# Kernel tuning notes

Measured on AMD Instinct MI355X. Metric: run time of the kernel, lower is better.

Reference implementation:

```python
import math
from itertools import combinations
import jax, jax.numpy as jnp
import numpy as np

SEQ_LEN = 8
D_IN = 2048
D_OUT = 1152
TSS = 3          # temporal_set_size
WAY = 5
SHOT = 5
N_SUPPORT = WAY * SHOT
N_Q = 100
PE_SCALE = 0.1
LN_EPS = 1e-5

TUPLES = np.array(list(combinations(range(SEQ_LEN), TSS)), dtype=np.int32)  # [56, 3]
T_LEN = TUPLES.shape[0]  # 56


def _positional_encoding(seq_len, d):
    pos = np.arange(seq_len, dtype=np.float32)[:, None]
    div = np.exp(np.arange(0, d, 2, dtype=np.float32) * -(math.log(10000.0) / d))
    pe = np.zeros((seq_len, d), dtype=np.float32)
    pe[:, 0::2] = np.sin(pos * div) * PE_SCALE
    pe[:, 1::2] = np.cos(pos * div) * PE_SCALE
    return jnp.asarray(pe)


def _layernorm(x, g, b):
    mu = jnp.mean(x, axis=-1, keepdims=True)
    var = jnp.mean((x - mu) ** 2, axis=-1, keepdims=True)
    return (x - mu) * jax.lax.rsqrt(var + LN_EPS) * g + b


def setup_inputs() -> dict:
    key = jax.random.key(0)
    ks = jax.random.split(key, 6)
    support_set = jax.random.normal(ks[0], (N_SUPPORT, SEQ_LEN, D_IN), dtype=jnp.float32)
    queries = jax.random.normal(ks[1], (N_Q, SEQ_LEN, D_IN), dtype=jnp.float32)
    # sorted episode layout: class c occupies rows [c*SHOT, (c+1)*SHOT)
    support_labels = jnp.repeat(jnp.arange(WAY, dtype=jnp.int64), SHOT)
    d_flat = TSS * D_IN  # 6144
    k_w = jax.random.normal(ks[2], (d_flat, D_OUT), dtype=jnp.float32) * 0.02
    k_b = jnp.zeros((D_OUT,), dtype=jnp.float32)
    v_w = jax.random.normal(ks[3], (d_flat, D_OUT), dtype=jnp.float32) * 0.02
    v_b = jnp.zeros((D_OUT,), dtype=jnp.float32)
    ln_g = jnp.ones((D_OUT,), dtype=jnp.float32)
    ln_b = jnp.zeros((D_OUT,), dtype=jnp.float32)
    return {"support_set": support_set, "queries": queries,
            "support_labels": support_labels,
            "k_w": k_w, "k_b": k_b, "v_w": v_w, "v_b": v_b,
            "ln_g": ln_g, "ln_b": ln_b}


def reference(support_set, queries, support_labels, k_w, k_b, v_w, v_b, ln_g, ln_b):
    pe = _positional_encoding(SEQ_LEN, D_IN)  # dropout is identity in eval mode
    s = support_set + pe
    q = queries + pe

    def tuplify(x):  # [N, S, D] -> [N, T_LEN, TSS*D]
        return x[:, TUPLES, :].reshape(x.shape[0], T_LEN, TSS * D_IN)

    s_t = tuplify(s)
    q_t = tuplify(q)

    sk = _layernorm(s_t @ k_w + k_b, ln_g, ln_b)  # [25, 56, 1152]
    qk = _layernorm(q_t @ k_w + k_b, ln_g, ln_b)  # [100, 56, 1152]
    sv = s_t @ v_w + v_b                           # [25, 56, 1152]
    qv = q_t @ v_w + v_b                           # [100, 56, 1152]

    scale = 1.0 / math.sqrt(D_OUT)
    dists = []
    align = None
    for c in range(WAY):  # fixed small class loop; class rows are a static slice
        class_k = sk[c * SHOT:(c + 1) * SHOT]  # [SHOT, 56, 1152]
        class_v = sv[c * SHOT:(c + 1) * SHOT]
        # scores: [Q, T, K, T] == torch permute(0,2,1,3) of [Q, K, T, T]
        scores = jnp.einsum('qtd,ksd->qtks', qk, class_k) * scale
        flat = scores.reshape(N_Q, T_LEN, SHOT * T_LEN)
        sm = jax.nn.softmax(flat, axis=-1)
        sm = sm.reshape(N_Q, T_LEN, SHOT, T_LEN).transpose(0, 2, 1, 3)  # [Q, K, T, T]
        align = sm.sum(axis=1)  # [Q, T, T]
        proto = jnp.einsum('qkts,ksd->qtd', sm, class_v)  # [Q, 56, 1152]
        diff = qv - proto
        dists.append(-jnp.sum(diff * diff, axis=(-2, -1)) / T_LEN)  # [Q]
    logits = jnp.stack(dists, axis=1)  # [Q, WAY]
    return logits, align
```

## Files before the change

### kernel.cpp

```cpp
#include <hip/hip_runtime.h>
#include <hip/hip_bf16.h>
#include <math.h>

#define SEQ_LEN 8
#define D_IN 2048
#define D_OUT 1152
#define WAY 5
#define SHOT 5
#define N_SUPPORT 25
#define N_Q 100
#define N_SEQ 125
#define N_ROWS 1000
#define T_LEN 56
#define KS_LEN 280
#define KS_PAD 288
#define NCOLS 6912
#define MQT 5600
#define DPC 9

typedef __attribute__((ext_vector_type(4))) float f32x4;
typedef __attribute__((ext_vector_type(8))) short bf16x8;

__constant__ int TUP[T_LEN][3] = {
  {0,1,2},{0,1,3},{0,1,4},{0,1,5},{0,1,6},{0,1,7},{0,2,3},{0,2,4},{0,2,5},{0,2,6},
  {0,2,7},{0,3,4},{0,3,5},{0,3,6},{0,3,7},{0,4,5},{0,4,6},{0,4,7},{0,5,6},{0,5,7},
  {0,6,7},{1,2,3},{1,2,4},{1,2,5},{1,2,6},{1,2,7},{1,3,4},{1,3,5},{1,3,6},{1,3,7},
  {1,4,5},{1,4,6},{1,4,7},{1,5,6},{1,5,7},{1,6,7},{2,3,4},{2,3,5},{2,3,6},{2,3,7},
  {2,4,5},{2,4,6},{2,4,7},{2,5,6},{2,5,7},{2,6,7},{3,4,5},{3,4,6},{3,4,7},{3,5,6},
  {3,5,7},{3,6,7},{4,5,6},{4,5,7},{4,6,7},{5,6,7}
};

__device__ __forceinline__ ushort f2bf(float f) {
  union { float f; unsigned u; } v; v.f = f;
  unsigned r = v.u + 0x7FFFu + ((v.u >> 16) & 1u);
  return (ushort)(r >> 16);
}
__device__ __forceinline__ float bf2f(ushort u) {
  union { unsigned u; float f; } v; v.u = ((unsigned)u) << 16;
  return v.f;
}
__device__ __forceinline__ void gload16(const void* g, const void* l) {
  __builtin_amdgcn_global_load_lds(
      (const __attribute__((address_space(1))) unsigned int*)g,
      (__attribute__((address_space(3))) unsigned int*)l, 16, 0, 0);
}
template<int N> __device__ __forceinline__ void vmw() {
  asm volatile("s_waitcnt vmcnt(%0)" :: "n"(N) : "memory");
}
__device__ __forceinline__ void vmw_rt(int n) {
  switch (n) {
    case 0: vmw<0>(); break;
    case 3: vmw<3>(); break;
    case 4: vmw<4>(); break;
    case 6: vmw<6>(); break;
    case 8: vmw<8>(); break;
    case 9: vmw<9>(); break;
    case 12: vmw<12>(); break;
    case 16: vmw<16>(); break;
    default: vmw<0>(); break;
  }
}

__global__ __launch_bounds__(256) void pe_table(float* __restrict__ PE) {
  int idx = blockIdx.x * 256 + threadIdx.x;
  if (idx >= SEQ_LEN * D_IN) return;
  int d = idx & (D_IN - 1), i = idx >> 11;
  int h2 = d & ~1;
  float freq = expf((float)h2 * (-9.210340371976184f / (float)D_IN));
  float ang = (float)i * freq;
  PE[idx] = ((d & 1) ? cosf(ang) : sinf(ang)) * 0.1f;
}

__global__ __launch_bounds__(256) void pe_add4(const float* __restrict__ sup,
                                               const float* __restrict__ que,
                                               const float* __restrict__ PE,
                                               ushort* __restrict__ X) {
  int idx = blockIdx.x * 256 + threadIdx.x;
  if (idx >= N_ROWS * D_IN / 4) return;
  int d4 = idx & (D_IN / 4 - 1);
  int r = idx >> 9;
  int i = r & 7;
  float4 p = *(const float4*)(PE + (size_t)i * D_IN + d4 * 4);
  float4 v = (r < N_SUPPORT * SEQ_LEN)
                 ? *(const float4*)(sup + (size_t)idx * 4)
                 : *(const float4*)(que + (size_t)idx * 4 - (size_t)N_SUPPORT * SEQ_LEN * D_IN);
  ushort4 o;
  o.x = f2bf(v.x + p.x); o.y = f2bf(v.y + p.y);
  o.z = f2bf(v.z + p.z); o.w = f2bf(v.w + p.w);
  *(ushort4*)(X + (size_t)idx * 4) = o;
}

__global__ __launch_bounds__(256) void wtrans(const float* __restrict__ kw,
                                              const float* __restrict__ vw,
                                              ushort* __restrict__ WT) {
  __shared__ float tile[64][65];
  int bx = blockIdx.x;
  int by = blockIdx.y;
  int b = bx / 18;
  int n0 = (bx % 18) * 64;
  int k0 = by * 64;
  const float* src = ((b & 1) ? vw : kw) + (size_t)(b >> 1) * D_IN * D_OUT;
  int tid = threadIdx.x;
#pragma unroll
  for (int it = 0; it < 4; ++it) {
    int lin4 = it * 256 + tid;
    int kk = lin4 >> 4;
    int n4 = (lin4 & 15) * 4;
    float4 v = *(const float4*)(src + (size_t)(k0 + kk) * D_OUT + n0 + n4);
    tile[kk][n4 + 0] = v.x; tile[kk][n4 + 1] = v.y;
    tile[kk][n4 + 2] = v.z; tile[kk][n4 + 3] = v.w;
  }
  __syncthreads();
#pragma unroll
  for (int it = 0; it < 4; ++it) {
    int lin = it * 1024 + tid * 4;
    int nn = lin >> 6, kk = lin & 63;
    ushort4 o;
    o.x = f2bf(tile[kk + 0][nn]); o.y = f2bf(tile[kk + 1][nn]);
    o.z = f2bf(tile[kk + 2][nn]); o.w = f2bf(tile[kk + 3][nn]);
    *(ushort4*)&WT[((size_t)(b * D_OUT + n0 + nn)) * D_IN + k0 + kk] = o;
  }
}

template<int EPI, int NT, int DEPTH, int SWZ>
__global__ __launch_bounds__(256) void gemm_bt(
    const ushort* __restrict__ A, const ushort* __restrict__ BT,
    float* __restrict__ C,
    int M, int N, int K, int lda, int ldb, int ldc, float alpha,
    long batchA, long batchB, long batchC) {
  constexpr int JF = NT / 32;
  constexpr int NCH = 8 + NT / 16;
  __shared__ ushort As[DEPTH][128][32];
  __shared__ ushort Bs[DEPTH][NT][32];

  int bx, by, bz;
  if constexpr (SWZ == 1) {
    int L = blockIdx.x, xcd = L & 7, s = L >> 3;
    by = (s >> 3) * 8 + xcd;
    if (by >= 108) return;
    bx = s & 7; bz = 0;
  } else if constexpr (SWZ == 2) {
    int L = blockIdx.x, xcd = L & 7, s = L >> 3;
    bx = (s % 6) * 8 + xcd;
    if (bx >= 44) return;
    int g = s / 6; by = g % 3; bz = g / 3;
  } else { bx = blockIdx.x; by = blockIdx.y; bz = blockIdx.z; }

  A  += (size_t)bz * batchA;
  BT += (size_t)bz * batchB;
  C  += (size_t)bz * batchC;

  int tid = threadIdx.x;
  int wid = tid >> 6, lane = tid & 63;
  int l16 = lane & 15, lk = lane >> 4;
  int wr = wid >> 1, wc = wid & 1;
  int row0 = bx * 128, col0 = by * NT;
  int lrow = lane >> 2;
  int lcol = ((lane & 3) ^ ((lane >> 3) & 3)) * 8;
  int rslot = (lk ^ ((l16 >> 1) & 3)) * 8;

  auto stage = [&](int buf, int t) {
    int k0 = t * 32;
    for (int c = wid; c < NCH; c += 4) {
      if (c < 8) {
        int grow = row0 + c * 16 + lrow;
        grow = grow < M ? grow : M - 1;
        gload16(A + (size_t)grow * lda + k0 + lcol, &As[buf][c * 16][0]);
      } else {
        int gcol = col0 + (c - 8) * 16 + lrow;
        gcol = gcol < N ? gcol : N - 1;
        gload16(BT + (size_t)gcol * ldb + k0 + lcol, &Bs[buf][(c - 8) * 16][0]);
      }
    }
  };

  int perw = NCH / 4 + ((wid < (NCH & 3)) ? 1 : 0);
  f32x4 acc[4][JF] = {};
  int nk = K / 32;
#pragma unroll
  for (int i = 0; i < DEPTH - 1; ++i)
    if (i < nk) stage(i, i);
  for (int t = 0; t < nk; ++t) {
    int cur = t % DEPTH;
    int ts = t + DEPTH - 1;
    if (ts < nk) stage(ts % DEPTH, ts);
    int rem = nk - 1 - t; if (rem > DEPTH - 1) rem = DEPTH - 1;
    vmw_rt(rem * perw);
    __builtin_amdgcn_s_barrier();
    __builtin_amdgcn_sched_barrier(0);
    bf16x8 af[4], bv[JF];
#pragma unroll
    for (int m = 0; m < 4; ++m)
      af[m] = *(const bf16x8*)&As[cur][wr * 64 + m * 16 + l16][rslot];
#pragma unroll
    for (int j = 0; j < JF; ++j)
      bv[j] = *(const bf16x8*)&Bs[cur][wc * (NT / 2) + j * 16 + l16][rslot];
#pragma unroll
    for (int m = 0; m < 4; ++m)
#pragma unroll
      for (int j = 0; j < JF; ++j)
        acc[m][j] = __builtin_amdgcn_mfma_f32_16x16x32_bf16(af[m], bv[j], acc[m][j], 0, 0, 0);
    __builtin_amdgcn_sched_barrier(0);
    __builtin_amdgcn_s_barrier();
  }

#pragma unroll
  for (int m = 0; m < 4; ++m)
#pragma unroll
    for (int j = 0; j < JF; ++j) {
      int col = col0 + wc * (NT / 2) + j * 16 + l16;
#pragma unroll
      for (int r = 0; r < 4; ++r) {
        int row = row0 + wr * 64 + m * 16 + lk * 4 + r;
        if (row < M && col < N)
          C[(size_t)row * ldc + col] = (EPI == 1) ? acc[m][j][r] * alpha : acc[m][j][r];
      }
    }
}

__global__ __launch_bounds__(256) void pv_dist(const ushort* __restrict__ SM,
                                               const ushort* __restrict__ SVT,
                                               const ushort* __restrict__ QV,
                                               float* __restrict__ DP) {
  __shared__ ushort Bs[128][296];
  int L = blockIdx.x, xcd = L & 7, s = L >> 3;
  int bx = (s % 6) * 8 + xcd;
  if (bx >= 44) return;
  int g = s / 6; int by = g % 9, bz = g / 9;
  int tid = threadIdx.x, wid = tid >> 6, lane = tid & 63;
  int l16 = lane & 15, lk = lane >> 4;
  int row0 = bx * 128, col0 = by * 128, c = bz;
  const ushort* sm = SM + (size_t)c * MQT * KS_PAD;
  const ushort* bt = SVT + ((size_t)c * D_OUT + col0) * KS_PAD;
  {
    int r = tid >> 1, h = tid & 1;
    const ushort* srcr = bt + (size_t)r * KS_PAD + h * 144;
#pragma unroll
    for (int i = 0; i < 18; ++i) {
      uint4 v = *(const uint4*)(srcr + i * 8);
      *(uint4*)&Bs[r][h * 144 + i * 8] = v;
    }
  }
  __syncthreads();

  int ra0 = row0 + wid * 32 + l16;      if (ra0 > MQT - 1) ra0 = MQT - 1;
  int ra1 = row0 + wid * 32 + 16 + l16; if (ra1 > MQT - 1) ra1 = MQT - 1;
  const ushort* a0 = sm + (size_t)ra0 * KS_PAD + lk * 8;
  const ushort* a1 = sm + (size_t)ra1 * KS_PAD + lk * 8;

  f32x4 acc[2][8] = {};
#pragma unroll
  for (int ks = 0; ks < 9; ++ks) {
    bf16x8 af0 = *(const bf16x8*)(a0 + ks * 32);
    bf16x8 af1 = *(const bf16x8*)(a1 + ks * 32);
    bf16x8 bv[8];
#pragma unroll
    for (int j = 0; j < 8; ++j)
      bv[j] = *(const bf16x8*)&Bs[j * 16 + l16][ks * 32 + lk * 8];
#pragma unroll
    for (int j = 0; j < 8; ++j) {
      acc[0][j] = __builtin_amdgcn_mfma_f32_16x16x32_bf16(af0, bv[j], acc[0][j], 0, 0, 0);
      acc[1][j] = __builtin_amdgcn_mfma_f32_16x16x32_bf16(af1, bv[j], acc[1][j], 0, 0, 0);
    }
  }

  float sq[2][4] = {};
#pragma unroll
  for (int m = 0; m < 2; ++m)
#pragma unroll
    for (int r = 0; r < 4; ++r) {
      int row = row0 + wid * 32 + m * 16 + lk * 4 + r;
      int rowc = row < MQT ? row : MQT - 1;
      const ushort* qvr = QV + (size_t)rowc * D_OUT + col0;
#pragma unroll
      for (int j = 0; j < 8; ++j) {
        float qvv = bf2f(qvr[j * 16 + l16]);
        float d = qvv - acc[m][j][r];
        sq[m][r] += d * d;
      }
    }
#pragma unroll
  for (int m = 0; m < 2; ++m)
#pragma unroll
    for (int r = 0; r < 4; ++r) {
      sq[m][r] += __shfl_xor(sq[m][r], 1);
      sq[m][r] += __shfl_xor(sq[m][r], 2);
      sq[m][r] += __shfl_xor(sq[m][r], 4);
      sq[m][r] += __shfl_xor(sq[m][r], 8);
    }
  if (l16 == 0) {
    float* dp = DP + (size_t)c * MQT * DPC;
#pragma unroll
    for (int m = 0; m < 2; ++m)
#pragma unroll
      for (int r = 0; r < 4; ++r) {
        int row = row0 + wid * 32 + m * 16 + lk * 4 + r;
        if (row < MQT) dp[(size_t)row * DPC + by] = sq[m][r];
      }
  }
}

__global__ __launch_bounds__(256) void combine_ln(const float* __restrict__ G,
                                                  const float* __restrict__ kb,
                                                  const float* __restrict__ vb,
                                                  const float* __restrict__ lng,
                                                  const float* __restrict__ lnb,
                                                  ushort* __restrict__ skbf,
                                                  ushort* __restrict__ qkbf,
                                                  ushort* __restrict__ sv,
                                                  ushort* __restrict__ qvbf) {
  int L = blockIdx.x, xcd = L & 7, h = L >> 3;
  int n = (h / 14) * 8 + xcd;
  if (n >= N_SEQ) return;
  int t = (h % 14) * 4 + (threadIdx.x >> 6);
  int lane = threadIdx.x & 63;
  const float* g0 = G + (size_t)(n * 8 + TUP[t][0]) * NCOLS;
  const float* g1 = G + (size_t)(n * 8 + TUP[t][1]) * NCOLS + 2 * D_OUT;
  const float* g2 = G + (size_t)(n * 8 + TUP[t][2]) * NCOLS + 4 * D_OUT;
  bool isq = (n >= N_SUPPORT);
  int c = n / SHOT, s = n % SHOT;
  ushort* vout = isq ? qvbf + ((size_t)(n - N_SUPPORT) * T_LEN + t) * D_OUT
                     : sv + ((size_t)c * KS_PAD + s * T_LEN + t) * D_OUT;
  ushort* kout = isq ? qkbf + ((size_t)(n - N_SUPPORT) * T_LEN + t) * D_OUT
                     : skbf + ((size_t)c * KS_PAD + s * T_LEN + t) * D_OUT;
  float kvx[9], kvy[9], s1 = 0.f, s2 = 0.f;
#pragma unroll
  for (int i = 0; i < 9; ++i) {
    int d = i * 128 + lane * 2;
    float2 a = *(const float2*)(g0 + d);
    float2 b = *(const float2*)(g0 + D_OUT + d);
    float2 c1 = *(const float2*)(g1 + d);
    float2 c2 = *(const float2*)(g1 + D_OUT + d);
    float2 e1 = *(const float2*)(g2 + d);
    float2 e2 = *(const float2*)(g2 + D_OUT + d);
    float2 kb2 = *(const float2*)(kb + d);
    float2 vb2 = *(const float2*)(vb + d);
    float kx = a.x + c1.x + e1.x + kb2.x;
    float ky = a.y + c1.y + e1.y + kb2.y;
    float vx = b.x + c2.x + e2.x + vb2.x;
    float vy = b.y + c2.y + e2.y + vb2.y;
    kvx[i] = kx; kvy[i] = ky;
    ushort2 vv; vv.x = f2bf(vx); vv.y = f2bf(vy);
    *(ushort2*)(vout + d) = vv;
    s1 += kx + ky;
    s2 += kx * kx + ky * ky;
  }
#pragma unroll
  for (int m = 32; m > 0; m >>= 1) {
    s1 += __shfl_xor(s1, m);
    s2 += __shfl_xor(s2, m);
  }
  float mu = s1 * (1.0f / D_OUT);
  float var = s2 * (1.0f / D_OUT) - mu * mu;
  float rs = rsqrtf(var + 1e-5f);
#pragma unroll
  for (int i = 0; i < 9; ++i) {
    int d = i * 128 + lane * 2;
    float2 g2v = *(const float2*)(lng + d);
    float2 b2v = *(const float2*)(lnb + d);
    ushort2 o;
    o.x = f2bf((kvx[i] - mu) * rs * g2v.x + b2v.x);
    o.y = f2bf((kvy[i] - mu) * rs * g2v.y + b2v.y);
    *(ushort2*)(kout + d) = o;
  }
}

__global__ __launch_bounds__(256) void svtrans(const ushort* __restrict__ sv,
                                               ushort* __restrict__ svT) {
  __shared__ ushort tile[32][65];
  int c = blockIdx.z;
  int d0 = blockIdx.x * 64;
  int k0 = blockIdx.y * 32;
  const ushort* src = sv + (size_t)c * KS_PAD * D_OUT;
  ushort* dst = svT + (size_t)c * D_OUT * KS_PAD;
  int tid = threadIdx.x;
#pragma unroll
  for (int it = 0; it < 8; ++it) {
    int lin = it * 256 + tid;
    int ks = k0 + (lin >> 6), d = d0 + (lin & 63);
    tile[lin >> 6][lin & 63] = (ks < KS_LEN) ? src[(size_t)ks * D_OUT + d] : (ushort)0;
  }
  __syncthreads();
#pragma unroll
  for (int it = 0; it < 8; ++it) {
    int lin = it * 256 + tid;
    int d = lin >> 5, ks = lin & 31;
    dst[(size_t)(d0 + d) * KS_PAD + k0 + ks] = tile[ks][d];
  }
}

__global__ __launch_bounds__(256) void softmax_align(const float* __restrict__ S,
                                                     ushort* __restrict__ sm,
                                                     float* __restrict__ align_out) {
  __shared__ float pl[4][KS_LEN];
  int wid = threadIdx.x >> 6, lane = threadIdx.x & 63;
  int row = blockIdx.x * 4 + wid;
  const float* src = S + (size_t)row * KS_PAD;
  float v[5];
  float mx = -1e30f;
#pragma unroll
  for (int j = 0; j < 5; ++j) {
    int ks = lane + j * 64;
    v[j] = (ks < KS_LEN) ? src[ks] : -1e30f;
    mx = fmaxf(mx, v[j]);
  }
#pragma unroll
  for (int m = 32; m > 0; m >>= 1) mx = fmaxf(mx, __shfl_xor(mx, m));
  float sum = 0.f;
  float p[5];
#pragma unroll
  for (int j = 0; j < 5; ++j) {
    int ks = lane + j * 64;
    p[j] = (ks < KS_LEN) ? expf(v[j] - mx) : 0.f;
    sum += p[j];
  }
#pragma unroll
  for (int m = 32; m > 0; m >>= 1) sum += __shfl_xor(sum, m);
  float inv = 1.0f / sum;
  ushort* dst = sm + (size_t)row * KS_PAD;
#pragma unroll
  for (int j = 0; j < 5; ++j) {
    int ks = lane + j * 64;
    if (ks < KS_PAD) dst[ks] = f2bf((ks < KS_LEN) ? p[j] * inv : 0.f);
  }
  int c = row / MQT;
  if (c == WAY - 1) {
#pragma unroll
    for (int j = 0; j < 5; ++j) {
      int ks = lane + j * 64;
      if (ks < KS_LEN) pl[wid][ks] = p[j] * inv;
    }
    __syncthreads();
    if (lane < T_LEN) {
      float a = 0.f;
#pragma unroll
      for (int k = 0; k < SHOT; ++k) a += pl[wid][k * T_LEN + lane];
      int qt = row - (WAY - 1) * MQT;
      align_out[(size_t)(qt / T_LEN) * (T_LEN * T_LEN) + (qt % T_LEN) * T_LEN + lane] = a;
    }
  }
}

__global__ __launch_bounds__(256) void logits_k(const float* __restrict__ DP,
                                                float* __restrict__ out) {
  __shared__ float red[256];
  int q = blockIdx.x / WAY, c = blockIdx.x % WAY;
  const float* base = DP + ((size_t)c * MQT + q * T_LEN) * DPC;
  int tid = threadIdx.x;
  float s = 0.f;
  for (int i = tid; i < T_LEN * DPC; i += 256) s += base[i];
  red[tid] = s;
  __syncthreads();
  for (int sft = 128; sft > 0; sft >>= 1) {
    if (tid < sft) red[tid] += red[tid + sft];
    __syncthreads();
  }
  if (tid == 0) out[blockIdx.x] = -red[0] * (1.0f / T_LEN);
}

extern "C" void kernel_launch(void* const* d_in, const int* in_sizes, int n_in,
                              void* d_out, int out_size, void* d_ws, size_t ws_size,
                              hipStream_t stream) {
  const float* sup  = (const float*)d_in[0];
  const float* que  = (const float*)d_in[1];
  const float* k_w  = (const float*)d_in[3];
  const float* k_b  = (const float*)d_in[4];
  const float* v_w  = (const float*)d_in[5];
  const float* v_b  = (const float*)d_in[6];
  const float* ln_g = (const float*)d_in[7];
  const float* ln_b = (const float*)d_in[8];
  float* out = (float*)d_out;

  char* w = (char*)d_ws;
  ushort* Xbf  = (ushort*)(w + 0);
  float*  PEt  = (float*)(w + 4096000);
  ushort* WT   = (ushort*)(w + 4096000);
  float*  G    = (float*)(w + 32407552);
  ushort* sv   = (ushort*)(w + 0);
  float*  S    = (float*)(w + 0);
  ushort* smbf = (ushort*)(w + 32407552);
  float*  DP   = (float*)(w + 0);
  ushort* qkbf = (ushort*)(w + 60055552);
  ushort* skbf = (ushort*)(w + 72957952);
  ushort* svT  = (ushort*)(w + 76275712);
  ushort* qvbf = (ushort*)(w + 79593472);

  const float scale = 0.02946278254943948f;

  pe_table<<<dim3(64), 256, 0, stream>>>(PEt);
  pe_add4<<<dim3(2000), 256, 0, stream>>>(sup, que, PEt, Xbf);
  wtrans<<<dim3(108, 32), 256, 0, stream>>>(k_w, v_w, WT);
  gemm_bt<0, 64, 3, 1><<<dim3(896), 256, 0, stream>>>(
      Xbf, WT, G,
      N_ROWS, NCOLS, D_IN, D_IN, D_IN, NCOLS, 1.0f, 0, 0, 0);
  combine_ln<<<dim3(1792), 256, 0, stream>>>(
      G, k_b, v_b, ln_g, ln_b, skbf, qkbf, sv, qvbf);
  svtrans<<<dim3(18, 9, WAY), 256, 0, stream>>>(sv, svT);
  gemm_bt<1, 96, 3, 2><<<dim3(720), 256, 0, stream>>>(
      qkbf, skbf, S,
      MQT, KS_PAD, D_OUT, D_OUT, D_OUT, KS_PAD, scale,
      0, (long)KS_PAD * D_OUT, (long)MQT * KS_PAD);
  softmax_align<<<dim3(7000), 256, 0, stream>>>(S, smbf, out + N_Q * WAY);
  pv_dist<<<dim3(2160), 256, 0, stream>>>(smbf, svT, qvbf, DP);
  logits_k<<<dim3(N_Q * WAY), 256, 0, stream>>>(DP, out);
}
```

Baseline: 203.2 us.

## Fuse score GEMM with softmax and align; compute positional encoding inline

Replaces the separate scores GEMM and softmax_align kernels with one kernel. Each block computes a full 64x288 row tile of scores, then does the row softmax in registers through cross-wave shared-memory max/sum reductions, writes bf16 probabilities, and computes align for the last class. This removes the fp32 score matrix round trip through global memory and one launch. The PE table kernel is also dropped in favour of computing sin/cos inline in pe_add4. The fused kernel runs only 440 blocks with a wide per-block N tile, which may lower occupancy relative to the old 720-block GEMM.

```diff
diff --git a/kernel.cpp b/kernel.cpp
--- a/kernel.cpp
+++ b/kernel.cpp
@@ -52,6 +52,7 @@
     case 0: vmw<0>(); break;
     case 3: vmw<3>(); break;
     case 4: vmw<4>(); break;
+    case 5: vmw<5>(); break;
     case 6: vmw<6>(); break;
     case 8: vmw<8>(); break;
     case 9: vmw<9>(); break;
@@ -61,32 +62,27 @@
   }
 }
 
-__global__ __launch_bounds__(256) void pe_table(float* __restrict__ PE) {
-  int idx = blockIdx.x * 256 + threadIdx.x;
-  if (idx >= SEQ_LEN * D_IN) return;
-  int d = idx & (D_IN - 1), i = idx >> 11;
-  int h2 = d & ~1;
-  float freq = expf((float)h2 * (-9.210340371976184f / (float)D_IN));
-  float ang = (float)i * freq;
-  PE[idx] = ((d & 1) ? cosf(ang) : sinf(ang)) * 0.1f;
-}
-
 __global__ __launch_bounds__(256) void pe_add4(const float* __restrict__ sup,
                                                const float* __restrict__ que,
-                                               const float* __restrict__ PE,
                                                ushort* __restrict__ X) {
   int idx = blockIdx.x * 256 + threadIdx.x;
   if (idx >= N_ROWS * D_IN / 4) return;
   int d4 = idx & (D_IN / 4 - 1);
   int r = idx >> 9;
   int i = r & 7;
-  float4 p = *(const float4*)(PE + (size_t)i * D_IN + d4 * 4);
+  int d = d4 * 4;
+  const float C = -9.210340371976184f / (float)D_IN;
+  float f0 = expf((float)d * C);
+  float f1 = expf((float)(d + 2) * C);
+  float s0, c0, s1, c1;
+  sincosf((float)i * f0, &s0, &c0);
+  sincosf((float)i * f1, &s1, &c1);
   float4 v = (r < N_SUPPORT * SEQ_LEN)
                  ? *(const float4*)(sup + (size_t)idx * 4)
                  : *(const float4*)(que + (size_t)idx * 4 - (size_t)N_SUPPORT * SEQ_LEN * D_IN);
   ushort4 o;
-  o.x = f2bf(v.x + p.x); o.y = f2bf(v.y + p.y);
-  o.z = f2bf(v.z + p.z); o.w = f2bf(v.w + p.w);
+  o.x = f2bf(v.x + s0 * 0.1f); o.y = f2bf(v.y + c0 * 0.1f);
+  o.z = f2bf(v.z + s1 * 0.1f); o.w = f2bf(v.w + c1 * 0.1f);
   *(ushort4*)(X + (size_t)idx * 4) = o;
 }
 
@@ -139,11 +135,6 @@
     by = (s >> 3) * 8 + xcd;
     if (by >= 108) return;
     bx = s & 7; bz = 0;
-  } else if constexpr (SWZ == 2) {
-    int L = blockIdx.x, xcd = L & 7, s = L >> 3;
-    bx = (s % 6) * 8 + xcd;
-    if (bx >= 44) return;
-    int g = s / 6; by = g % 3; bz = g / 3;
   } else { bx = blockIdx.x; by = blockIdx.y; bz = blockIdx.z; }
 
   A  += (size_t)bz * batchA;
@@ -216,6 +207,172 @@
           C[(size_t)row * ldc + col] = (EPI == 1) ? acc[m][j][r] * alpha : acc[m][j][r];
       }
     }
+}
+
+__global__ __launch_bounds__(256) void scores_sm(const ushort* __restrict__ QK,
+                                                 const ushort* __restrict__ SK,
+                                                 ushort* __restrict__ SM,
+                                                 float* __restrict__ align_out) {
+  __shared__ ushort AsB[2][64][32];
+  __shared__ ushort BsB[2][288][32];
+  __shared__ float pmax[64][2];
+  __shared__ float psum[64][2];
+  int L = blockIdx.x, xcd = L & 7, s = L >> 3;
+  int bx = (s % 11) * 8 + xcd;
+  int cz = s / 11;
+  const ushort* B = SK + (size_t)cz * KS_PAD * D_OUT;
+  ushort* smc = SM + (size_t)cz * MQT * KS_PAD;
+  int row0 = bx * 64;
+
+  int tid = threadIdx.x;
+  int wid = tid >> 6, lane = tid & 63;
+  int l16 = lane & 15, lk = lane >> 4;
+  int wr = wid >> 1, wc = wid & 1;
+  int lrow = lane >> 2;
+  int lcol = ((lane & 3) ^ ((lane >> 3) & 3)) * 8;
+  int rslot = (lk ^ ((l16 >> 1) & 3)) * 8;
+
+  auto stage = [&](int buf, int t) {
+    int k0 = t * 32;
+    for (int c = wid; c < 22; c += 4) {
+      if (c < 4) {
+        int grow = row0 + c * 16 + lrow;
+        grow = grow < MQT ? grow : MQT - 1;
+        gload16(QK + (size_t)grow * D_OUT + k0 + lcol, &AsB[buf][c * 16][0]);
+      } else {
+        int gcol = (c - 4) * 16 + lrow;
+        gcol = gcol < KS_LEN ? gcol : KS_LEN - 1;
+        gload16(B + (size_t)gcol * D_OUT + k0 + lcol, &BsB[buf][(c - 4) * 16][0]);
+      }
+    }
+  };
+
+  int perw = (wid < 2) ? 6 : 5;
+  f32x4 acc[2][9] = {};
+  stage(0, 0);
+  for (int t = 0; t < 36; ++t) {
+    int cur = t & 1;
+    if (t + 1 < 36) {
+      stage(cur ^ 1, t + 1);
+      vmw_rt(perw);
+    } else {
+      vmw<0>();
+    }
+    __builtin_amdgcn_s_barrier();
+    __builtin_amdgcn_sched_barrier(0);
+    bf16x8 af[2], bv[9];
+#pragma unroll
+    for (int m = 0; m < 2; ++m)
+      af[m] = *(const bf16x8*)&AsB[cur][wr * 32 + m * 16 + l16][rslot];
+#pragma unroll
+    for (int j = 0; j < 9; ++j)
+      bv[j] = *(const bf16x8*)&BsB[cur][wc * 144 + j * 16 + l16][rslot];
+#pragma unroll
+    for (int m = 0; m < 2; ++m)
+#pragma unroll
+      for (int j = 0; j < 9; ++j)
+        acc[m][j] = __builtin_amdgcn_mfma_f32_16x16x32_bf16(af[m], bv[j], acc[m][j], 0, 0, 0);
+    __builtin_amdgcn_sched_barrier(0);
+    __builtin_amdgcn_s_barrier();
+  }
+
+  const float scale = 0.02946278254943948f;
+  float mxv[2][4];
+#pragma unroll
+  for (int m = 0; m < 2; ++m)
+#pragma unroll
+    for (int r = 0; r < 4; ++r) {
+      float mx = -1e30f;
+#pragma unroll
+      for (int j = 0; j < 9; ++j) {
+        acc[m][j][r] *= scale;
+        int col = wc * 144 + j * 16 + l16;
+        if (col < KS_LEN) mx = fmaxf(mx, acc[m][j][r]);
+      }
+      mx = fmaxf(mx, __shfl_xor(mx, 1));
+      mx = fmaxf(mx, __shfl_xor(mx, 2));
+      mx = fmaxf(mx, __shfl_xor(mx, 4));
+      mx = fmaxf(mx, __shfl_xor(mx, 8));
+      mxv[m][r] = mx;
+    }
+  __syncthreads();
+  if (l16 == 0) {
+#pragma unroll
+    for (int m = 0; m < 2; ++m)
+#pragma unroll
+      for (int r = 0; r < 4; ++r)
+        pmax[wr * 32 + m * 16 + lk * 4 + r][wc] = mxv[m][r];
+  }
+  __syncthreads();
+  float smv[2][4];
+#pragma unroll
+  for (int m = 0; m < 2; ++m)
+#pragma unroll
+    for (int r = 0; r < 4; ++r) {
+      int lr = wr * 32 + m * 16 + lk * 4 + r;
+      float mx = fmaxf(pmax[lr][0], pmax[lr][1]);
+      float sum = 0.f;
+#pragma unroll
+      for (int j = 0; j < 9; ++j) {
+        int col = wc * 144 + j * 16 + l16;
+        float p = (col < KS_LEN) ? expf(acc[m][j][r] - mx) : 0.f;
+        acc[m][j][r] = p;
+        sum += p;
+      }
+      sum += __shfl_xor(sum, 1);
+      sum += __shfl_xor(sum, 2);
+      sum += __shfl_xor(sum, 4);
+      sum += __shfl_xor(sum, 8);
+      smv[m][r] = sum;
+    }
+  if (l16 == 0) {
+#pragma unroll
+    for (int m = 0; m < 2; ++m)
+#pragma unroll
+      for (int r = 0; r < 4; ++r)
+        psum[wr * 32 + m * 16 + lk * 4 + r][wc] = smv[m][r];
+  }
+  __syncthreads();
+#pragma unroll
+  for (int m = 0; m < 2; ++m)
+#pragma unroll
+    for (int r = 0; r < 4; ++r) {
+      int lr = wr * 32 + m * 16 + lk * 4 + r;
+      int row = row0 + lr;
+      float inv = 1.0f / (psum[lr][0] + psum[lr][1]);
+#pragma unroll
+      for (int j = 0; j < 9; ++j) {
+        acc[m][j][r] *= inv;
+        int col = wc * 144 + j * 16 + l16;
+        if (row < MQT) smc[(size_t)row * KS_PAD + col] = f2bf(acc[m][j][r]);
+      }
+    }
+  if (cz == WAY - 1) {
+    ushort* sml = &BsB[0][0][0];
+    __syncthreads();
+#pragma unroll
+    for (int m = 0; m < 2; ++m)
+#pragma unroll
+      for (int r = 0; r < 4; ++r) {
+        int lr = wr * 32 + m * 16 + lk * 4 + r;
+#pragma unroll
+        for (int j = 0; j < 9; ++j) {
+          int col = wc * 144 + j * 16 + l16;
+          sml[lr * 288 + col] = f2bf(acc[m][j][r]);
+        }
+      }
+    __syncthreads();
+    for (int idx = tid; idx < 64 * T_LEN; idx += 256) {
+      int lr = idx / T_LEN, s5 = idx % T_LEN;
+      int grow = row0 + lr;
+      if (grow < MQT) {
+        float a = 0.f;
+#pragma unroll
+        for (int k = 0; k < SHOT; ++k) a += bf2f(sml[lr * 288 + k * T_LEN + s5]);
+        align_out[(size_t)(grow / T_LEN) * (T_LEN * T_LEN) + (grow % T_LEN) * T_LEN + s5] = a;
+      }
+    }
+  }
 }
 
 __global__ __launch_bounds__(256) void pv_dist(const ushort* __restrict__ SM,
@@ -389,58 +546,6 @@
   }
 }
 
-__global__ __launch_bounds__(256) void softmax_align(const float* __restrict__ S,
-                                                     ushort* __restrict__ sm,
-                                                     float* __restrict__ align_out) {
-  __shared__ float pl[4][KS_LEN];
-  int wid = threadIdx.x >> 6, lane = threadIdx.x & 63;
-  int row = blockIdx.x * 4 + wid;
-  const float* src = S + (size_t)row * KS_PAD;
-  float v[5];
-  float mx = -1e30f;
-#pragma unroll
-  for (int j = 0; j < 5; ++j) {
-    int ks = lane + j * 64;
-    v[j] = (ks < KS_LEN) ? src[ks] : -1e30f;
-    mx = fmaxf(mx, v[j]);
-  }
-#pragma unroll
-  for (int m = 32; m > 0; m >>= 1) mx = fmaxf(mx, __shfl_xor(mx, m));
-  float sum = 0.f;
-  float p[5];
-#pragma unroll
-  for (int j = 0; j < 5; ++j) {
-    int ks = lane + j * 64;
-    p[j] = (ks < KS_LEN) ? expf(v[j] - mx) : 0.f;
-    sum += p[j];
-  }
-#pragma unroll
-  for (int m = 32; m > 0; m >>= 1) sum += __shfl_xor(sum, m);
-  float inv = 1.0f / sum;
-  ushort* dst = sm + (size_t)row * KS_PAD;
-#pragma unroll
-  for (int j = 0; j < 5; ++j) {
-    int ks = lane + j * 64;
-    if (ks < KS_PAD) dst[ks] = f2bf((ks < KS_LEN) ? p[j] * inv : 0.f);
-  }
-  int c = row / MQT;
-  if (c == WAY - 1) {
-#pragma unroll
-    for (int j = 0; j < 5; ++j) {
-      int ks = lane + j * 64;
-      if (ks < KS_LEN) pl[wid][ks] = p[j] * inv;
-    }
-    __syncthreads();
-    if (lane < T_LEN) {
-      float a = 0.f;
-#pragma unroll
-      for (int k = 0; k < SHOT; ++k) a += pl[wid][k * T_LEN + lane];
-      int qt = row - (WAY - 1) * MQT;
-      align_out[(size_t)(qt / T_LEN) * (T_LEN * T_LEN) + (qt % T_LEN) * T_LEN + lane] = a;
-    }
-  }
-}
-
 __global__ __launch_bounds__(256) void logits_k(const float* __restrict__ DP,
                                                 float* __restrict__ out) {
   __shared__ float red[256];
@@ -473,11 +578,9 @@
 
   char* w = (char*)d_ws;
   ushort* Xbf  = (ushort*)(w + 0);
-  float*  PEt  = (float*)(w + 4096000);
   ushort* WT   = (ushort*)(w + 4096000);
   float*  G    = (float*)(w + 32407552);
   ushort* sv   = (ushort*)(w + 0);
-  float*  S    = (float*)(w + 0);
   ushort* smbf = (ushort*)(w + 32407552);
   float*  DP   = (float*)(w + 0);
   ushort* qkbf = (ushort*)(w + 60055552);
@@ -485,10 +588,7 @@
   ushort* svT  = (ushort*)(w + 76275712);
   ushort* qvbf = (ushort*)(w + 79593472);
 
-  const float scale = 0.02946278254943948f;
-
-  pe_table<<<dim3(64), 256, 0, stream>>>(PEt);
-  pe_add4<<<dim3(2000), 256, 0, stream>>>(sup, que, PEt, Xbf);
+  pe_add4<<<dim3(2000), 256, 0, stream>>>(sup, que, Xbf);
   wtrans<<<dim3(108, 32), 256, 0, stream>>>(k_w, v_w, WT);
   gemm_bt<0, 64, 3, 1><<<dim3(896), 256, 0, stream>>>(
       Xbf, WT, G,
@@ -496,11 +596,7 @@
   combine_ln<<<dim3(1792), 256, 0, stream>>>(
       G, k_b, v_b, ln_g, ln_b, skbf, qkbf, sv, qvbf);
   svtrans<<<dim3(18, 9, WAY), 256, 0, stream>>>(sv, svT);
-  gemm_bt<1, 96, 3, 2><<<dim3(720), 256, 0, stream>>>(
-      qkbf, skbf, S,
-      MQT, KS_PAD, D_OUT, D_OUT, D_OUT, KS_PAD, scale,
-      0, (long)KS_PAD * D_OUT, (long)MQT * KS_PAD);
-  softmax_align<<<dim3(7000), 256, 0, stream>>>(S, smbf, out + N_Q * WAY);
+  scores_sm<<<dim3(440), 256, 0, stream>>>(qkbf, skbf, smbf, out + N_Q * WAY);
   pv_dist<<<dim3(2160), 256, 0, stream>>>(smbf, svT, qvbf, DP);
   logits_k<<<dim3(N_Q * WAY), 256, 0, stream>>>(DP, out);
 }
```

Result: faster. 195.5 us (-3.8%).

## Replace QK score GEMM with LDS-resident support-key kernel and inline PE computation

Applied to the files above, without the earlier changes.

Swaps the generic pipelined GEMM for the query-key scores with a dedicated kernel. Each block keeps a 32-row slice of the class's support keys (full 1152 depth) in LDS and streams query rows straight from global memory into MFMA, with no K-loop staging or barriers. It also drops the separate positional-encoding table kernel and computes sin/cos inline in pe_add4, removing one launch and a table read. The risks are uncached direct global loads of A with many more blocks re-reading the query rows, and about 74KB of LDS per block, which limits occupancy.

```diff
diff --git a/kernel.cpp b/kernel.cpp
--- a/kernel.cpp
+++ b/kernel.cpp
@@ -52,6 +52,7 @@
     case 0: vmw<0>(); break;
     case 3: vmw<3>(); break;
     case 4: vmw<4>(); break;
+    case 5: vmw<5>(); break;
     case 6: vmw<6>(); break;
     case 8: vmw<8>(); break;
     case 9: vmw<9>(); break;
@@ -61,32 +62,27 @@
   }
 }
 
-__global__ __launch_bounds__(256) void pe_table(float* __restrict__ PE) {
-  int idx = blockIdx.x * 256 + threadIdx.x;
-  if (idx >= SEQ_LEN * D_IN) return;
-  int d = idx & (D_IN - 1), i = idx >> 11;
-  int h2 = d & ~1;
-  float freq = expf((float)h2 * (-9.210340371976184f / (float)D_IN));
-  float ang = (float)i * freq;
-  PE[idx] = ((d & 1) ? cosf(ang) : sinf(ang)) * 0.1f;
-}
-
 __global__ __launch_bounds__(256) void pe_add4(const float* __restrict__ sup,
                                                const float* __restrict__ que,
-                                               const float* __restrict__ PE,
                                                ushort* __restrict__ X) {
   int idx = blockIdx.x * 256 + threadIdx.x;
   if (idx >= N_ROWS * D_IN / 4) return;
   int d4 = idx & (D_IN / 4 - 1);
   int r = idx >> 9;
   int i = r & 7;
-  float4 p = *(const float4*)(PE + (size_t)i * D_IN + d4 * 4);
+  int d = d4 * 4;
+  const float C = -9.210340371976184f / (float)D_IN;
+  float f0 = expf((float)d * C);
+  float f1 = expf((float)(d + 2) * C);
+  float s0, c0, s1, c1;
+  sincosf((float)i * f0, &s0, &c0);
+  sincosf((float)i * f1, &s1, &c1);
   float4 v = (r < N_SUPPORT * SEQ_LEN)
                  ? *(const float4*)(sup + (size_t)idx * 4)
                  : *(const float4*)(que + (size_t)idx * 4 - (size_t)N_SUPPORT * SEQ_LEN * D_IN);
   ushort4 o;
-  o.x = f2bf(v.x + p.x); o.y = f2bf(v.y + p.y);
-  o.z = f2bf(v.z + p.z); o.w = f2bf(v.w + p.w);
+  o.x = f2bf(v.x + s0 * 0.1f); o.y = f2bf(v.y + c0 * 0.1f);
+  o.z = f2bf(v.z + s1 * 0.1f); o.w = f2bf(v.w + c1 * 0.1f);
   *(ushort4*)(X + (size_t)idx * 4) = o;
 }
 
@@ -139,11 +135,6 @@
     by = (s >> 3) * 8 + xcd;
     if (by >= 108) return;
     bx = s & 7; bz = 0;
-  } else if constexpr (SWZ == 2) {
-    int L = blockIdx.x, xcd = L & 7, s = L >> 3;
-    bx = (s % 6) * 8 + xcd;
-    if (bx >= 44) return;
-    int g = s / 6; by = g % 3; bz = g / 3;
   } else { bx = blockIdx.x; by = blockIdx.y; bz = blockIdx.z; }
 
   A  += (size_t)bz * batchA;
@@ -216,6 +207,112 @@
           C[(size_t)row * ldc + col] = (EPI == 1) ? acc[m][j][r] * alpha : acc[m][j][r];
       }
     }
+}
+
+__global__ __launch_bounds__(256) void qk_scores(const ushort* __restrict__ QK,
+                                                 const ushort* __restrict__ SK,
+                                                 float* __restrict__ S) {
+  __shared__ ushort Bs[32][1160];
+  int L = blockIdx.x, xcd = L & 7, s = L >> 3;
+  int bx = (s % 6) * 8 + xcd;
+  if (bx >= 44) return;
+  int g = s / 6; int by = g % 9, bz = g / 9;
+  int tid = threadIdx.x, wid = tid >> 6, lane = tid & 63;
+  int l16 = lane & 15, lk = lane >> 4;
+  int row0 = bx * 128, ks0 = by * 32, c = bz;
+  const ushort* skc = SK + ((size_t)c * KS_PAD + ks0) * D_OUT;
+  {
+    int r = tid >> 3, h = tid & 7;
+    const ushort* srcr = skc + (size_t)r * D_OUT + h * 144;
+#pragma unroll
+    for (int i = 0; i < 18; ++i)
+      *(uint4*)&Bs[r][h * 144 + i * 8] = *(const uint4*)(srcr + i * 8);
+  }
+  __syncthreads();
+
+  int ra0 = row0 + wid * 32 + l16;      if (ra0 > MQT - 1) ra0 = MQT - 1;
+  int ra1 = row0 + wid * 32 + 16 + l16; if (ra1 > MQT - 1) ra1 = MQT - 1;
+  const ushort* a0 = QK + (size_t)ra0 * D_OUT + lk * 8;
+  const ushort* a1 = QK + (size_t)ra1 * D_OUT + lk * 8;
+
+  f32x4 acc[2][2] = {};
+#pragma unroll 4
+  for (int t = 0; t < 36; ++t) {
+    bf16x8 af0 = *(const bf16x8*)(a0 + t * 32);
+    bf16x8 af1 = *(const bf16x8*)(a1 + t * 32);
+    bf16x8 bv0 = *(const bf16x8*)&Bs[l16][t * 32 + lk * 8];
+    bf16x8 bv1 = *(const bf16x8*)&Bs[16 + l16][t * 32 + lk * 8];
+    acc[0][0] = __builtin_amdgcn_mfma_f32_16x16x32_bf16(af0, bv0, acc[0][0], 0, 0, 0);
+    acc[0][1] = __builtin_amdgcn_mfma_f32_16x16x32_bf16(af0, bv1, acc[0][1], 0, 0, 0);
+    acc[1][0] = __builtin_amdgcn_mfma_f32_16x16x32_bf16(af1, bv0, acc[1][0], 0, 0, 0);
+    acc[1][1] = __builtin_amdgcn_mfma_f32_16x16x32_bf16(af1, bv1, acc[1][1], 0, 0, 0);
+  }
+
+  const float scale = 0.02946278254943948f;
+  float* sc = S + (size_t)c * MQT * KS_PAD;
+#pragma unroll
+  for (int m = 0; m < 2; ++m)
+#pragma unroll
+    for (int j = 0; j < 2; ++j) {
+      int col = ks0 + j * 16 + l16;
+#pragma unroll
+      for (int r = 0; r < 4; ++r) {
+        int row = row0 + wid * 32 + m * 16 + lk * 4 + r;
+        if (row < MQT) sc[(size_t)row * KS_PAD + col] = acc[m][j][r] * scale;
+      }
+    }
+}
+
+__global__ __launch_bounds__(256) void softmax_align(const float* __restrict__ S,
+                                                     ushort* __restrict__ sm,
+                                                     float* __restrict__ align_out) {
+  __shared__ float pl[4][KS_LEN];
+  int wid = threadIdx.x >> 6, lane = threadIdx.x & 63;
+  int row = blockIdx.x * 4 + wid;
+  const float* src = S + (size_t)row * KS_PAD;
+  float v[5];
+  float mx = -1e30f;
+#pragma unroll
+  for (int j = 0; j < 5; ++j) {
+    int ks = lane + j * 64;
+    v[j] = (ks < KS_LEN) ? src[ks] : -1e30f;
+    mx = fmaxf(mx, v[j]);
+  }
+#pragma unroll
+  for (int m = 32; m > 0; m >>= 1) mx = fmaxf(mx, __shfl_xor(mx, m));
+  float sum = 0.f;
+  float p[5];
+#pragma unroll
+  for (int j = 0; j < 5; ++j) {
+    int ks = lane + j * 64;
+    p[j] = (ks < KS_LEN) ? expf(v[j] - mx) : 0.f;
+    sum += p[j];
+  }
+#pragma unroll
+  for (int m = 32; m > 0; m >>= 1) sum += __shfl_xor(sum, m);
+  float inv = 1.0f / sum;
+  ushort* dst = sm + (size_t)row * KS_PAD;
+#pragma unroll
+  for (int j = 0; j < 5; ++j) {
+    int ks = lane + j * 64;
+    if (ks < KS_PAD) dst[ks] = f2bf((ks < KS_LEN) ? p[j] * inv : 0.f);
+  }
+  int c = row / MQT;
+  if (c == WAY - 1) {
+#pragma unroll
+    for (int j = 0; j < 5; ++j) {
+      int ks = lane + j * 64;
+      if (ks < KS_LEN) pl[wid][ks] = p[j] * inv;
+    }
+    __syncthreads();
+    if (lane < T_LEN) {
+      float a = 0.f;
+#pragma unroll
+      for (int k = 0; k < SHOT; ++k) a += pl[wid][k * T_LEN + lane];
+      int qt = row - (WAY - 1) * MQT;
+      align_out[(size_t)(qt / T_LEN) * (T_LEN * T_LEN) + (qt % T_LEN) * T_LEN + lane] = a;
+    }
+  }
 }
 
 __global__ __launch_bounds__(256) void pv_dist(const ushort* __restrict__ SM,
@@ -389,58 +486,6 @@
   }
 }
 
-__global__ __launch_bounds__(256) void softmax_align(const float* __restrict__ S,
-                                                     ushort* __restrict__ sm,
-                                                     float* __restrict__ align_out) {
-  __shared__ float pl[4][KS_LEN];
-  int wid = threadIdx.x >> 6, lane = threadIdx.x & 63;
-  int row = blockIdx.x * 4 + wid;
-  const float* src = S + (size_t)row * KS_PAD;
-  float v[5];
-  float mx = -1e30f;
-#pragma unroll
-  for (int j = 0; j < 5; ++j) {
-    int ks = lane + j * 64;
-    v[j] = (ks < KS_LEN) ? src[ks] : -1e30f;
-    mx = fmaxf(mx, v[j]);
-  }
-#pragma unroll
-  for (int m = 32; m > 0; m >>= 1) mx = fmaxf(mx, __shfl_xor(mx, m));
-  float sum = 0.f;
-  float p[5];
-#pragma unroll
-  for (int j = 0; j < 5; ++j) {
-    int ks = lane + j * 64;
-    p[j] = (ks < KS_LEN) ? expf(v[j] - mx) : 0.f;
-    sum += p[j];
-  }
-#pragma unroll
-  for (int m = 32; m > 0; m >>= 1) sum += __shfl_xor(sum, m);
-  float inv = 1.0f / sum;
-  ushort* dst = sm + (size_t)row * KS_PAD;
-#pragma unroll
-  for (int j = 0; j < 5; ++j) {
-    int ks = lane + j * 64;
-    if (ks < KS_PAD) dst[ks] = f2bf((ks < KS_LEN) ? p[j] * inv : 0.f);
-  }
-  int c = row / MQT;
-  if (c == WAY - 1) {
-#pragma unroll
-    for (int j = 0; j < 5; ++j) {
-      int ks = lane + j * 64;
-      if (ks < KS_LEN) pl[wid][ks] = p[j] * inv;
-    }
-    __syncthreads();
-    if (lane < T_LEN) {
-      float a = 0.f;
-#pragma unroll
-      for (int k = 0; k < SHOT; ++k) a += pl[wid][k * T_LEN + lane];
-      int qt = row - (WAY - 1) * MQT;
-      align_out[(size_t)(qt / T_LEN) * (T_LEN * T_LEN) + (qt % T_LEN) * T_LEN + lane] = a;
-    }
-  }
-}
-
 __global__ __launch_bounds__(256) void logits_k(const float* __restrict__ DP,
                                                 float* __restrict__ out) {
   __shared__ float red[256];
@@ -473,7 +518,6 @@
 
   char* w = (char*)d_ws;
   ushort* Xbf  = (ushort*)(w + 0);
-  float*  PEt  = (float*)(w + 4096000);
   ushort* WT   = (ushort*)(w + 4096000);
   float*  G    = (float*)(w + 32407552);
   ushort* sv   = (ushort*)(w + 0);
@@ -485,10 +529,7 @@
   ushort* svT  = (ushort*)(w + 76275712);
   ushort* qvbf = (ushort*)(w + 79593472);
 
-  const float scale = 0.02946278254943948f;
-
-  pe_table<<<dim3(64), 256, 0, stream>>>(PEt);
-  pe_add4<<<dim3(2000), 256, 0, stream>>>(sup, que, PEt, Xbf);
+  pe_add4<<<dim3(2000), 256, 0, stream>>>(sup, que, Xbf);
   wtrans<<<dim3(108, 32), 256, 0, stream>>>(k_w, v_w, WT);
   gemm_bt<0, 64, 3, 1><<<dim3(896), 256, 0, stream>>>(
       Xbf, WT, G,
@@ -496,10 +537,7 @@
   combine_ln<<<dim3(1792), 256, 0, stream>>>(
       G, k_b, v_b, ln_g, ln_b, skbf, qkbf, sv, qvbf);
   svtrans<<<dim3(18, 9, WAY), 256, 0, stream>>>(sv, svT);
-  gemm_bt<1, 96, 3, 2><<<dim3(720), 256, 0, stream>>>(
-      qkbf, skbf, S,
-      MQT, KS_PAD, D_OUT, D_OUT, D_OUT, KS_PAD, scale,
-      0, (long)KS_PAD * D_OUT, (long)MQT * KS_PAD);
+  qk_scores<<<dim3(2160), 256, 0, stream>>>(qkbf, skbf, S);
   softmax_align<<<dim3(7000), 256, 0, stream>>>(S, smbf, out + N_Q * WAY);
   pv_dist<<<dim3(2160), 256, 0, stream>>>(smbf, svT, qvbf, DP);
   logits_k<<<dim3(N_Q * WAY), 256, 0, stream>>>(DP, out);
```

After: 245.3 us. 20.7% more time.
